# Kernel tuning notes

Hardware: AMD Instinct MI355X
Metric: run time of the kernel (lower is better)

## Reference

```python
import jax, jax.numpy as jnp
import numpy as np

EPS = 1e-8  # torch F.cosine_similarity eps


def _cos_attn_masked(x, roi, h):
    """Replicates MultiHeadedAttention_2: per-head cosine similarity, relu,
    global top-k(4) column mask (torch advanced-indexing semantics), roi mask.
    x: (B,num,C), roi: (B,num,num). Returns (B,num,num,h)."""
    B, num, C = x.shape
    dk = C // h
    xh = x.reshape(B, num, h, dk)
    n = jnp.linalg.norm(xh, axis=-1)                       # (B,num,h)
    dots = jnp.einsum('bihd,bjhd->bijh', xh, xh)           # (B,i,j,h)
    denom = jnp.maximum(n[:, :, None, :] * n[:, None, :, :], EPS)
    a = jax.nn.relu(dots / denom)                          # (B,i,j,h)
    # torch: values, idces = topk(attn, 4, dim=2); atten_mask[:, :, idces, :] = 1
    # -> column j is unmasked iff j appears ANYWHERE in idces (global union).
    _, idx = jax.lax.top_k(jnp.moveaxis(a, 2, -1), 4)      # (B,i,h,4) over j
    vec = jnp.zeros((num,), a.dtype).at[idx.reshape(-1)].set(1.0)
    return a * roi[:, :, :, None] * vec[None, None, :, None]


def _gconv_relu(x, w, b):
    """Grouped 1x1 Conv1d + ReLU. x: (B,C,num), w: (g, co_g, ci_g), b: (co,)."""
    B, C, num = x.shape
    g, co_g, ci_g = w.shape
    xg = x.reshape(B, g, ci_g, num)
    y = jnp.einsum('goc,bgcn->bgon', w, xg).reshape(B, g * co_g, num)
    return jax.nn.relu(y + b[None, :, None])


def setup_inputs() -> dict:
    key = jax.random.key(0)
    ks = jax.random.split(key, 10)
    B, num = 4, 1024
    c_in, c_mid, c_out, group = 256, 256, 256, 4
    inp = {
        'input': jax.random.normal(ks[0], (B, num, c_in), jnp.float32),
        'masks_roi': jax.random.randint(ks[1], (B, num, num), 0, 2, jnp.int32),
        'score_mask': jax.random.randint(ks[2], (B, num), 0, 2, jnp.int32),
        'gt_feat': jax.random.normal(ks[3], (B, num, c_in), jnp.float32),
        'w1': jax.random.normal(ks[4], (group, c_mid // group, c_in // group), jnp.float32) * 0.05,
        'b1': jax.random.normal(ks[5], (c_mid,), jnp.float32) * 0.05,
        'w2': jax.random.normal(ks[6], (group, c_out // group, c_mid // group), jnp.float32) * 0.05,
        'b2': jax.random.normal(ks[7], (c_out,), jnp.float32) * 0.05,
        'gt_w': jax.random.normal(ks[8], (c_out, c_in), jnp.float32) * 0.05,
        'gt_b': jax.random.normal(ks[9], (c_out,), jnp.float32) * 0.05,
        # module init explicitly zeroes LayerNorm weight AND bias
        'ln_w': jnp.zeros((c_out,), jnp.float32),
        'ln_b': jnp.zeros((c_out,), jnp.float32),
        'multi_head': 4,
    }
    return inp


def reference(input, masks_roi, score_mask, gt_feat, w1, b1, w2, b2, gt_w, gt_b, ln_w, ln_b, multi_head):
    h = multi_head
    B, num, C = input.shape
    dt = input.dtype
    sm = score_mask.astype(dt)
    roi = masks_roi.astype(dt) * sm[:, None, :]
    f_mask = jax.vmap(jnp.diag)((sm == 0).astype(dt))      # (B,num,num)

    gts = jax.nn.relu(gt_feat @ gt_w.T + gt_b).reshape(B, -1, gt_w.shape[0])

    # --- stage 1 ---
    a1 = (_cos_attn_masked(input, roi, h) + f_mask[:, :, :, None]) / 4.0
    p1 = a1.transpose(0, 3, 2, 1)                          # (B,h,j,i)
    out1 = _gconv_relu(input.transpose(0, 2, 1), w1, b1)   # (B,mid,num)
    mid = out1.shape[1]
    o1m = jnp.einsum('bhcj,bhji->bhci', out1.reshape(B, h, mid // h, num), p1)
    out1 = out1 + o1m.reshape(B, mid, num)

    # --- stage 2 ---
    a2 = (_cos_attn_masked(out1.transpose(0, 2, 1), roi, h) + f_mask[:, :, :, None]) / 4.0
    p2 = a2.transpose(0, 3, 2, 1)
    out2 = _gconv_relu(out1, w2, b2)                       # (B,out,num)
    co = out2.shape[1]
    o2m = jnp.einsum('bhcj,bhji->bhci', out2.reshape(B, h, co // h, num), p2)
    y = o2m.reshape(B, co, num).transpose(0, 2, 1)         # (B,num,out)

    # LayerNorm(eps=1e-6) -- weight/bias zero-initialized per the module
    mu = y.mean(-1, keepdims=True)
    var = y.var(-1, keepdims=True)
    node_feat = (y - mu) / jnp.sqrt(var + 1e-6) * ln_w + ln_b

    out2 = out2 + node_feat.transpose(0, 2, 1)
    return out2.transpose(0, 2, 1), gts, node_feat


if __name__ == '__main__':
    o = reference(**setup_inputs())
    print([x.shape for x in o])
```

## Files before the change

kernel.cpp:

```cpp
#include <hip/hip_runtime.h>
#include <hip/hip_bf16.h>

#define B_    4
#define NUM   1024
#define CH    256
#define HEADS 4
#define DK    64
#define LDK   72
#define NJC   4

typedef __hip_bfloat16 bf;
typedef __attribute__((ext_vector_type(8))) short short8;
typedef __attribute__((ext_vector_type(4))) float f32x4;
typedef unsigned long long u64;
typedef unsigned u32;

#define SEG_ ((size_t)B_ * NUM * CH)

__device__ inline bf tobf(float v) { return __float2bfloat16(v); }

__device__ inline void stage_tile(const float* __restrict__ src, size_t row0,
                                  int col0, int rowstride, bf (*dst)[LDK], int tid) {
  int r = tid >> 4, c4 = (tid & 15) * 4;
  #pragma unroll
  for (int it = 0; it < 4; ++it) {
    int row = r + it * 16;
    const float4 v = *(const float4*)&src[(row0 + row) * (size_t)rowstride + col0 + c4];
    union { bf h4[4]; short4 s4; } u;
    u.h4[0] = tobf(v.x); u.h4[1] = tobf(v.y); u.h4[2] = tobf(v.z); u.h4[3] = tobf(v.w);
    *(short4*)&dst[row][c4] = u.s4;
  }
}

__device__ inline void load_afrag_bf(const bf* __restrict__ arow, int quad, short8 af[2]) {
  af[0] = *(const short8*)&arow[quad * 8];
  af[1] = *(const short8*)&arow[32 + quad * 8];
}

__device__ inline u32 umax(u32 a, u32 b) { return a > b ? a : b; }
__device__ inline u32 umin(u32 a, u32 b) { return a < b ? a : b; }

__device__ inline void sort4(u32& k0, u32& k1, u32& k2, u32& k3) {
  u32 h;
  h = umax(k0, k1); k1 = umin(k0, k1); k0 = h;
  h = umax(k2, k3); k3 = umin(k2, k3); k2 = h;
  h = umax(k0, k2); k2 = umin(k0, k2); k0 = h;
  h = umax(k1, k3); k3 = umin(k1, k3); k1 = h;
  h = umax(k1, k2); k2 = umin(k1, k2); k1 = h;
}

__device__ inline void merge4(u32 t[4], u32 o0, u32 o1, u32 o2, u32 o3) {
  u32 m0 = umax(t[0], o3), m1 = umax(t[1], o2);
  u32 m2 = umax(t[2], o1), m3 = umax(t[3], o0);
  u32 h;
  h = umax(m0, m2); m2 = umin(m0, m2); m0 = h;
  h = umax(m1, m3); m3 = umin(m1, m3); m1 = h;
  h = umax(m0, m1); m1 = umin(m0, m1); m0 = h;
  h = umax(m2, m3); m3 = umin(m2, m3); m2 = h;
  t[0] = m0; t[1] = m1; t[2] = m2; t[3] = m3;
}

__device__ inline void conv_body(
    char* SM, int m0, int g, int tid,
    const float* __restrict__ x, const float* __restrict__ parts,
    const float* __restrict__ w,
    const float* __restrict__ bias, const int* __restrict__ smask,
    float seedbase, bool skipx, float* __restrict__ out, float* __restrict__ out2,
    float* __restrict__ rn, bf* __restrict__ xbf) {
  float (*Xs)[65] = (float(*)[65])SM;
  float (*Wsm)[65] = (float(*)[65])(SM + 16640);
  const int tx = tid & 15, ty = tid >> 4;
  #pragma unroll
  for (int l = 0; l < 16; ++l) {
    int idx = tid + l * 256; int r = idx >> 6, c = idx & 63;
    size_t gi = (size_t)(m0 + r) * CH + g * DK + c;
    float v = x[gi];
    if (parts)
      v += parts[gi] + parts[SEG_ + gi] + parts[2 * SEG_ + gi] + parts[3 * SEG_ + gi];
    Xs[r][c] = v;
    Wsm[r][c] = w[g * DK * DK + r * DK + c];
  }
  __syncthreads();
  if (!skipx) {
    int r = tid >> 4, c4 = (tid & 15) * 4;
    #pragma unroll
    for (int it = 0; it < 4; ++it) {
      int row = r + it * 16;
      union { bf h4[4]; short4 s4; } u;
      u.h4[0] = tobf(Xs[row][c4]);     u.h4[1] = tobf(Xs[row][c4 + 1]);
      u.h4[2] = tobf(Xs[row][c4 + 2]); u.h4[3] = tobf(Xs[row][c4 + 3]);
      *(short4*)&xbf[(size_t)(m0 + row) * CH + g * DK + c4] = u.s4;
    }
  }
  if (!skipx) {
    int wv = tid >> 6, lane = tid & 63;
    int row = wv * 16 + (lane >> 2), part = lane & 3;
    float s = 0.f;
    #pragma unroll
    for (int k = 0; k < 16; ++k) {
      float v = Xs[row][part * 16 + k];
      s += v * v;
    }
    s += __shfl_xor(s, 1, 64);
    s += __shfl_xor(s, 2, 64);
    if (part == 0)
      rn[(size_t)(m0 + row) * HEADS + g] = 1.0f / fmaxf(sqrtf(s), 1e-4f);
  }
  float acc[4][4] = {};
  #pragma unroll 8
  for (int k = 0; k < DK; ++k) {
    float av[4], bv[4];
    #pragma unroll
    for (int i = 0; i < 4; ++i) av[i] = Xs[ty * 4 + i][k];
    #pragma unroll
    for (int j = 0; j < 4; ++j) bv[j] = Wsm[tx * 4 + j][k];
    #pragma unroll
    for (int i = 0; i < 4; ++i)
      #pragma unroll
      for (int j = 0; j < 4; ++j) acc[i][j] += av[i] * bv[j];
  }
  #pragma unroll
  for (int i = 0; i < 4; ++i) {
    int row = m0 + ty * 4 + i;
    float seed = seedbase + ((smask[row] == 0) ? 0.25f : 0.f);
    #pragma unroll
    for (int j = 0; j < 4; ++j) {
      int o = g * DK + tx * 4 + j;
      size_t idx = (size_t)row * CH + o;
      float v = fmaxf(acc[i][j] + bias[o], 0.f);
      out[idx] = v;
      out2[idx] = v * seed;
    }
  }
}

__device__ inline void gts_body(
    char* SM, int m0, int n0, int tid,
    const float* __restrict__ gf, const float* __restrict__ gw,
    const float* __restrict__ gb, float* __restrict__ out) {
  bf (*As)[LDK] = (bf(*)[LDK])SM;
  bf (*Bs)[LDK] = (bf(*)[LDK])(SM + 9216);
  const int lane = tid & 63, w = tid >> 6;
  const int m = lane & 15, quad = lane >> 4;
  f32x4 acc[4] = {{0.f,0.f,0.f,0.f},{0.f,0.f,0.f,0.f},{0.f,0.f,0.f,0.f},{0.f,0.f,0.f,0.f}};
  for (int k0 = 0; k0 < 256; k0 += 64) {
    __syncthreads();
    stage_tile(gf, m0, k0, 256, As, tid);
    stage_tile(gw, n0, k0, 256, Bs, tid);
    __syncthreads();
    #pragma unroll
    for (int kb = 0; kb < 2; ++kb) {
      short8 a = *(const short8*)&As[w * 16 + m][kb * 32 + quad * 8];
      #pragma unroll
      for (int nt = 0; nt < 4; ++nt) {
        short8 bb = *(const short8*)&Bs[nt * 16 + m][kb * 32 + quad * 8];
        acc[nt] = __builtin_amdgcn_mfma_f32_16x16x32_bf16(a, bb, acc[nt], 0, 0, 0);
      }
    }
  }
  #pragma unroll
  for (int nt = 0; nt < 4; ++nt)
    #pragma unroll
    for (int r = 0; r < 4; ++r) {
      int row = m0 + w * 16 + quad * 4 + r, col = n0 + nt * 16 + m;
      out[(size_t)row * 256 + col] = fmaxf(acc[nt][r] + gb[col], 0.f);
    }
}

__device__ inline void pack_body(int blkrow, int tid, const int* __restrict__ mroi,
                                 const int* __restrict__ smask, u64* __restrict__ pk,
                                 float* __restrict__ v1, float* __restrict__ v2) {
  if (blkrow < 4) {
    int i = blkrow * 256 + tid;
    v1[i] = 0.f; v2[i] = 0.f;
  }
  int row = blkrow * 4 + (tid >> 6);
  int lane = tid & 63;
  int b = row >> 10;
  const int* mr = &mroi[(size_t)row * NUM];
  const int* sm = &smask[b * NUM];
  #pragma unroll
  for (int wd = 0; wd < 16; ++wd) {
    int j = wd * 64 + lane;
    u64 word = __ballot((mr[j] != 0) && (sm[j] != 0));
    if (lane == 0) pk[(size_t)row * 16 + wd] = word;
  }
}

__global__ __launch_bounds__(256) void head_kernel(
    const float* __restrict__ x, const float* __restrict__ w1,
    const float* __restrict__ b1, const int* __restrict__ smask,
    float* __restrict__ X1, float* __restrict__ F1, float* __restrict__ rn,
    bf* __restrict__ xbf,
    const float* __restrict__ gf, const float* __restrict__ gw,
    const float* __restrict__ gb, float* __restrict__ gts_out,
    const int* __restrict__ mroi, u64* __restrict__ pk,
    float* __restrict__ v1, float* __restrict__ v2,
    const float* __restrict__ lnw, const float* __restrict__ lnb,
    u32* __restrict__ lnz) {
  __shared__ __align__(16) char SM[33280];
  __shared__ u64 bz[4];
  const int tid = threadIdx.x;
  if (blockIdx.y < 4) {
    conv_body(SM, blockIdx.x * 64, blockIdx.y, tid, x, nullptr, w1, b1, smask,
              1.0f, false, X1, F1, rn, xbf);
  } else if (blockIdx.y < 8) {
    gts_body(SM, blockIdx.x * 64, (blockIdx.y - 4) * 64, tid, gf, gw, gb, gts_out);
  } else {
    int blkrow = (blockIdx.y - 8) * 64 + blockIdx.x;
    pack_body(blkrow, tid, mroi, smask, pk, v1, v2);
    if (blkrow == 4) {
      bool nz = (lnw[tid] != 0.f) || (lnb[tid] != 0.f);
      u64 wb = __ballot(nz);
      if ((tid & 63) == 0) bz[tid >> 6] = wb;
      __syncthreads();
      if (tid == 0) *lnz = ((bz[0] | bz[1] | bz[2] | bz[3]) == 0ull) ? 1u : 0u;
    }
  }
}

__global__ __launch_bounds__(256) void conv_kernel(
    const float* __restrict__ x, const float* __restrict__ parts,
    const float* __restrict__ w,
    const float* __restrict__ bias, const int* __restrict__ smask,
    float seedbase, float* __restrict__ out, float* __restrict__ out2,
    float* __restrict__ rn, bf* __restrict__ xbf, const u32* __restrict__ lnz) {
  __shared__ __align__(16) char SM[33280];
  bool skipx = (lnz != nullptr) && (*lnz != 0u);
  conv_body(SM, blockIdx.x * 64, blockIdx.y, threadIdx.x, x, parts, w, bias, smask,
            seedbase, skipx, out, out2, rn, xbf);
}

__global__ __launch_bounds__(1024, 4) void score_topk_kernel(
    const bf* __restrict__ xbf, const float* __restrict__ rn,
    const u64* __restrict__ pk, bf* __restrict__ wsout,
    float* __restrict__ vec, const u32* __restrict__ lnz) {
  if (lnz != nullptr && *lnz != 0u) return;
  __shared__ __align__(16) bf Xj[2][4][64][LDK];
  __shared__ u32 cexch[3][64][4];
  const int b = blockIdx.z, h = blockIdx.y, it = blockIdx.x;
  const int i0 = it * 64;
  const int tid = threadIdx.x, lane = tid & 63, wv = tid >> 6;
  const int m = lane & 15, quad = lane >> 4;
  const int g4 = wv >> 2, rw = wv & 3;
  const int slot = tid & 511, srow = slot >> 3, schunk = slot & 7;
  const int tpair = tid >> 9;

  auto sload = [&](int k, short8& n0, short8& n1) {
    size_t base = (size_t)b * NUM;
    int t0 = (tpair * 2 + 0) * 4 + k, t1 = (tpair * 2 + 1) * 4 + k;
    n0 = *(const short8*)&xbf[(base + t0 * 64 + srow) * CH + h * DK + schunk * 8];
    n1 = *(const short8*)&xbf[(base + t1 * 64 + srow) * CH + h * DK + schunk * 8];
  };
  auto swrite = [&](int buf, short8 n0, short8 n1) {
    *(short8*)&Xj[buf][tpair * 2 + 0][srow][schunk * 8] = n0;
    *(short8*)&Xj[buf][tpair * 2 + 1][srow][schunk * 8] = n1;
  };

  {
    short8 n0, n1;
    sload(0, n0, n1);
    swrite(0, n0, n1);
  }

  short8 afrag[2];
  load_afrag_bf(&xbf[((size_t)b * NUM + i0 + rw * 16 + m) * CH + h * DK], quad, afrag);

  u32 keys[4][4] = {};

  const int row0 = i0 + rw * 16 + quad * 4;
  bf* wpb = wsout + ((size_t)(b * HEADS + h) * NUM + row0) * NUM + m;
  const u64* pkb = pk + ((size_t)b * NUM + row0) * 16;
  const float* rnp = rn + ((size_t)b * NUM + m) * HEADS + h;

  __syncthreads();

  #pragma unroll
  for (int k = 0; k < 4; ++k) {
    const int cur = k & 1;
    const int jt = g4 * 4 + k;
    const int j0 = jt * 64;
    short8 n0, n1;
    if (k < 3) sload(k + 1, n0, n1);
    u64 wrm[4];
    float rnj4[4];
    #pragma unroll
    for (int r = 0; r < 4; ++r)
      wrm[r] = pkb[r * 16 + jt] >> m;
    #pragma unroll
    for (int nt = 0; nt < 4; ++nt)
      rnj4[nt] = rnp[(j0 + nt * 16) * HEADS];

    f32x4 acc[4];
    #pragma unroll
    for (int nt = 0; nt < 4; ++nt) {
      acc[nt] = (f32x4){0.f, 0.f, 0.f, 0.f};
      #pragma unroll
      for (int kb = 0; kb < 2; ++kb) {
        short8 bb = *(const short8*)&Xj[cur][g4][nt * 16 + m][kb * 32 + quad * 8];
        acc[nt] = __builtin_amdgcn_mfma_f32_16x16x32_bf16(afrag[kb], bb, acc[nt], 0, 0, 0);
      }
    }
    const u32 jinv0 = 1023u - (u32)(j0 + m);
    #pragma unroll
    for (int r = 0; r < 4; ++r) {
      float kv0 = fmaxf(acc[0][r] * rnj4[0], 0.f);
      float kv1 = fmaxf(acc[1][r] * rnj4[1], 0.f);
      float kv2 = fmaxf(acc[2][r] * rnj4[2], 0.f);
      float kv3 = fmaxf(acc[3][r] * rnj4[3], 0.f);
      u32 k0 = (__float_as_uint(kv0) & 0xFFFFFC00u) | jinv0;
      u32 k1 = (__float_as_uint(kv1) & 0xFFFFFC00u) | (jinv0 - 16u);
      u32 k2 = (__float_as_uint(kv2) & 0xFFFFFC00u) | (jinv0 - 32u);
      u32 k3 = (__float_as_uint(kv3) & 0xFFFFFC00u) | (jinv0 - 48u);
      sort4(k0, k1, k2, k3);
      merge4(keys[r], k0, k1, k2, k3);
      wpb[r * NUM + j0 +  0] = tobf((wrm[r] &        1ull) ? kv0 : 0.f);
      wpb[r * NUM + j0 + 16] = tobf((wrm[r] >> 16 &  1ull) ? kv1 : 0.f);
      wpb[r * NUM + j0 + 32] = tobf((wrm[r] >> 32 &  1ull) ? kv2 : 0.f);
      wpb[r * NUM + j0 + 48] = tobf((wrm[r] >> 48 &  1ull) ? kv3 : 0.f);
    }
    if (k < 3) swrite(cur ^ 1, n0, n1);
    __syncthreads();
  }

  #pragma unroll
  for (int st = 1; st < 16; st <<= 1) {
    #pragma unroll
    for (int r = 0; r < 4; ++r) {
      u32 o0 = (u32)__shfl_xor((int)keys[r][0], st, 64);
      u32 o1 = (u32)__shfl_xor((int)keys[r][1], st, 64);
      u32 o2 = (u32)__shfl_xor((int)keys[r][2], st, 64);
      u32 o3 = (u32)__shfl_xor((int)keys[r][3], st, 64);
      merge4(keys[r], o0, o1, o2, o3);
    }
  }
  if (g4 != 0 && m == 0) {
    #pragma unroll
    for (int r = 0; r < 4; ++r) {
      int rl = rw * 16 + quad * 4 + r;
      #pragma unroll
      for (int q = 0; q < 4; ++q) cexch[g4 - 1][rl][q] = keys[r][q];
    }
  }
  __syncthreads();
  if (g4 == 0 && m == 0) {
    #pragma unroll
    for (int r = 0; r < 4; ++r) {
      int rl = rw * 16 + quad * 4 + r;
      merge4(keys[r], cexch[0][rl][0], cexch[0][rl][1], cexch[0][rl][2], cexch[0][rl][3]);
      merge4(keys[r], cexch[1][rl][0], cexch[1][rl][1], cexch[1][rl][2], cexch[1][rl][3]);
      merge4(keys[r], cexch[2][rl][0], cexch[2][rl][1], cexch[2][rl][2], cexch[2][rl][3]);
      #pragma unroll
      for (int q = 0; q < 4; ++q)
        vec[1023u - (keys[r][q] & 0x3FFu)] = 1.0f;
    }
  }
}

__global__ __launch_bounds__(256) void pv_kernel(
    const bf* __restrict__ wsin, const float* __restrict__ conv,
    const float* __restrict__ rn, const float* __restrict__ vec,
    float* __restrict__ outp, const u32* __restrict__ lnz) {
  if (lnz != nullptr && *lnz != 0u) return;
  __shared__ __align__(16) bf Cv[2][64][LDK];
  const int b = blockIdx.z, h = blockIdx.y;
  const int it = blockIdx.x >> 2, jc = blockIdx.x & 3;
  const int i0 = it * 64, jbase = jc * 256;
  const int tid = threadIdx.x, lane = tid & 63, w = tid >> 6;
  const int m = lane & 15, quad = lane >> 4;
  const int jr = tid >> 4, c4 = tid & 15;

  float rni4[4];
  #pragma unroll
  for (int r = 0; r < 4; ++r)
    rni4[r] = 0.25f * rn[((size_t)b * NUM + i0 + w * 16 + quad * 4 + r) * HEADS + h];

  const size_t wsrow = ((size_t)(b * HEADS + h) * NUM + i0 + w * 16 + m) * NUM + jbase;

  f32x4 om[4] = {{0.f,0.f,0.f,0.f},{0.f,0.f,0.f,0.f},{0.f,0.f,0.f,0.f},{0.f,0.f,0.f,0.f}};

  float4 pre[4]; float psc[4];
  auto issue = [&](int jt) {
    #pragma unroll
    for (int itt = 0; itt < 4; ++itt) {
      int j = jbase + jt * 64 + jr + itt * 16;
      psc[itt] = vec[j];
      pre[itt] = *(const float4*)&conv[((size_t)b * NUM + j) * CH + h * DK + c4 * 4];
    }
  };
  auto lwrite = [&](int buf) {
    #pragma unroll
    for (int itt = 0; itt < 4; ++itt) {
      int j = jr + itt * 16;
      Cv[buf][c4 * 4 + 0][j] = tobf(pre[itt].x * psc[itt]);
      Cv[buf][c4 * 4 + 1][j] = tobf(pre[itt].y * psc[itt]);
      Cv[buf][c4 * 4 + 2][j] = tobf(pre[itt].z * psc[itt]);
      Cv[buf][c4 * 4 + 3][j] = tobf(pre[itt].w * psc[itt]);
    }
  };

  issue(0); lwrite(0);
  short8 a0 = *(const short8*)&wsin[wsrow + quad * 8];
  short8 a1 = *(const short8*)&wsin[wsrow + 32 + quad * 8];

  for (int jt = 0; jt < 4; ++jt) {
    const int cur = jt & 1;
    short8 na0, na1;
    if (jt < 3) {
      issue(jt + 1);
      na0 = *(const short8*)&wsin[wsrow + (jt + 1) * 64 + quad * 8];
      na1 = *(const short8*)&wsin[wsrow + (jt + 1) * 64 + 32 + quad * 8];
    }
    __syncthreads();
    #pragma unroll
    for (int ct = 0; ct < 4; ++ct)
      om[ct] = __builtin_amdgcn_mfma_f32_16x16x32_bf16(
          a0, *(const short8*)&Cv[cur][ct * 16 + m][quad * 8], om[ct], 0, 0, 0);
    #pragma unroll
    for (int ct = 0; ct < 4; ++ct)
      om[ct] = __builtin_amdgcn_mfma_f32_16x16x32_bf16(
          a1, *(const short8*)&Cv[cur][ct * 16 + m][32 + quad * 8], om[ct], 0, 0, 0);
    if (jt < 3) { lwrite(cur ^ 1); a0 = na0; a1 = na1; }
  }

  const size_t ob = (size_t)(jc * B_ + b) * NUM;
  #pragma unroll
  for (int ct = 0; ct < 4; ++ct)
    #pragma unroll
    for (int r = 0; r < 4; ++r) {
      size_t idx = (ob + i0 + w * 16 + quad * 4 + r) * CH + h * DK + ct * 16 + m;
      outp[idx] = om[ct][r] * rni4[r];
    }
}

__global__ __launch_bounds__(256) void final_kernel(
    float* __restrict__ ybnf, float* __restrict__ out0,
    const float* __restrict__ lnw, const float* __restrict__ lnb,
    const float* __restrict__ parts, const u32* __restrict__ lnz) {
  int bn = blockIdx.x;
  int c = threadIdx.x;
  size_t idx = (size_t)bn * CH + c;
  if (lnz != nullptr && *lnz != 0u) {
    ybnf[idx] = 0.f;
    return;
  }
  __shared__ float r1[4];
  __shared__ float r2[4];
  float y = ybnf[idx] + parts[idx] + parts[SEG_ + idx]
          + parts[2 * SEG_ + idx] + parts[3 * SEG_ + idx];
  float x2v = out0[idx];
  float s = y;
  #pragma unroll
  for (int off = 32; off; off >>= 1) s += __shfl_down(s, off, 64);
  int wave = c >> 6, lane = c & 63;
  if (lane == 0) r1[wave] = s;
  __syncthreads();
  float mu = (r1[0] + r1[1] + r1[2] + r1[3]) * (1.f / 256.f);
  float d = y - mu;
  float s2 = d * d;
  #pragma unroll
  for (int off = 32; off; off >>= 1) s2 += __shfl_down(s2, off, 64);
  if (lane == 0) r2[wave] = s2;
  __syncthreads();
  float var = (r2[0] + r2[1] + r2[2] + r2[3]) * (1.f / 256.f);
  float nf = d * rsqrtf(var + 1e-6f) * lnw[c] + lnb[c];
  ybnf[idx] = nf;
  out0[idx] = x2v + nf;
}

extern "C" void kernel_launch(void* const* d_in, const int* in_sizes, int n_in,
                              void* d_out, int out_size, void* d_ws, size_t ws_size,
                              hipStream_t stream) {
  const float* input = (const float*)d_in[0];
  const int* mroi = (const int*)d_in[1];
  const int* smask = (const int*)d_in[2];
  const float* gt_feat = (const float*)d_in[3];
  const float* w1 = (const float*)d_in[4];
  const float* b1 = (const float*)d_in[5];
  const float* w2 = (const float*)d_in[6];
  const float* b2 = (const float*)d_in[7];
  const float* gt_w = (const float*)d_in[8];
  const float* gt_b = (const float*)d_in[9];
  const float* lnw = (const float*)d_in[10];
  const float* lnb = (const float*)d_in[11];

  const size_t SEG = SEG_;
  float* out0 = (float*)d_out;
  float* gts = out0 + SEG;
  float* nfreg = out0 + 2 * SEG;

  float* F1 = (float*)d_ws;
  float* RN = F1 + SEG;
  float* VEC1 = RN + (size_t)B_ * NUM * HEADS;
  float* VEC2 = VEC1 + NUM;
  u64* PK = (u64*)(VEC2 + NUM);
  bf* XBF = (bf*)(PK + (size_t)B_ * NUM * 16);
  bf* WSC = XBF + SEG;
  float* P = (float*)(WSC + (size_t)B_ * HEADS * NUM * NUM);
  u32* LNZ = (u32*)(P + 4 * SEG);

  float* X1 = nfreg;
  float* X2 = out0;
  float* Yb = nfreg;

  head_kernel<<<dim3(64, 24), 256, 0, stream>>>(
      input, w1, b1, smask, X1, F1, RN, XBF,
      gt_feat, gt_w, gt_b, gts, mroi, PK, VEC1, VEC2, lnw, lnb, LNZ);

  score_topk_kernel<<<dim3(16, HEADS, B_), 1024, 0, stream>>>(
      XBF, RN, PK, WSC, VEC1, nullptr);
  pv_kernel<<<dim3(16 * NJC, HEADS, B_), 256, 0, stream>>>(WSC, X1, RN, VEC1, P, nullptr);

  conv_kernel<<<dim3(64, 4), 256, 0, stream>>>(F1, P, w2, b2, smask, 0.0f, X2, Yb, RN, XBF, LNZ);
  score_topk_kernel<<<dim3(16, HEADS, B_), 1024, 0, stream>>>(
      XBF, RN, PK, WSC, VEC2, LNZ);
  pv_kernel<<<dim3(16 * NJC, HEADS, B_), 256, 0, stream>>>(WSC, X2, RN, VEC2, P, LNZ);

  final_kernel<<<4096, 256, 0, stream>>>(Yb, X2, lnw, lnb, P, LNZ);
}
```

Before: 162.6 us.

## Stage all j-tiles in LDS upfront and drop per-iteration barriers in score_topk

The score/top-k kernel now loads all 16 j-tiles of the head slice into shared memory at once, replacing the double-buffered per-iteration loads. This removes the four per-iteration __syncthreads and the load/compute interleave, in exchange for much larger LDS use (about 147KB for Xj) and so lower occupancy, plus more live registers during the upfront load. Separately, the conv kernel skips writing out2 when the skip flag is set.

Result: slower. 166.9 us (+2.6%).

```diff
diff --git a/kernel.cpp b/kernel.cpp
--- a/kernel.cpp
+++ b/kernel.cpp
@@ -129,7 +129,7 @@
       size_t idx = (size_t)row * CH + o;
       float v = fmaxf(acc[i][j] + bias[o], 0.f);
       out[idx] = v;
-      out2[idx] = v * seed;
+      if (!skipx) out2[idx] = v * seed;
     }
   }
 }
@@ -236,7 +236,7 @@
     const u64* __restrict__ pk, bf* __restrict__ wsout,
     float* __restrict__ vec, const u32* __restrict__ lnz) {
   if (lnz != nullptr && *lnz != 0u) return;
-  __shared__ __align__(16) bf Xj[2][4][64][LDK];
+  __shared__ __align__(16) bf Xj[16][64][LDK];
   __shared__ u32 cexch[3][64][4];
   const int b = blockIdx.z, h = blockIdx.y, it = blockIdx.x;
   const int i0 = it * 64;
@@ -246,21 +246,15 @@
   const int slot = tid & 511, srow = slot >> 3, schunk = slot & 7;
   const int tpair = tid >> 9;
 
-  auto sload = [&](int k, short8& n0, short8& n1) {
-    size_t base = (size_t)b * NUM;
-    int t0 = (tpair * 2 + 0) * 4 + k, t1 = (tpair * 2 + 1) * 4 + k;
-    n0 = *(const short8*)&xbf[(base + t0 * 64 + srow) * CH + h * DK + schunk * 8];
-    n1 = *(const short8*)&xbf[(base + t1 * 64 + srow) * CH + h * DK + schunk * 8];
-  };
-  auto swrite = [&](int buf, short8 n0, short8 n1) {
-    *(short8*)&Xj[buf][tpair * 2 + 0][srow][schunk * 8] = n0;
-    *(short8*)&Xj[buf][tpair * 2 + 1][srow][schunk * 8] = n1;
-  };
-
   {
-    short8 n0, n1;
-    sload(0, n0, n1);
-    swrite(0, n0, n1);
+    short8 v[8];
+    const bf* sb = &xbf[((size_t)b * NUM + srow) * CH + h * DK + schunk * 8];
+    #pragma unroll
+    for (int q = 0; q < 8; ++q)
+      v[q] = *(const short8*)&sb[(size_t)(tpair + 2 * q) * 64 * CH];
+    #pragma unroll
+    for (int q = 0; q < 8; ++q)
+      *(short8*)&Xj[tpair + 2 * q][srow][schunk * 8] = v[q];
   }
 
   short8 afrag[2];
@@ -277,11 +271,8 @@
 
   #pragma unroll
   for (int k = 0; k < 4; ++k) {
-    const int cur = k & 1;
     const int jt = g4 * 4 + k;
     const int j0 = jt * 64;
-    short8 n0, n1;
-    if (k < 3) sload(k + 1, n0, n1);
     u64 wrm[4];
     float rnj4[4];
     #pragma unroll
@@ -297,7 +288,7 @@
       acc[nt] = (f32x4){0.f, 0.f, 0.f, 0.f};
       #pragma unroll
       for (int kb = 0; kb < 2; ++kb) {
-        short8 bb = *(const short8*)&Xj[cur][g4][nt * 16 + m][kb * 32 + quad * 8];
+        short8 bb = *(const short8*)&Xj[jt][nt * 16 + m][kb * 32 + quad * 8];
         acc[nt] = __builtin_amdgcn_mfma_f32_16x16x32_bf16(afrag[kb], bb, acc[nt], 0, 0, 0);
       }
     }
@@ -319,8 +310,6 @@
       wpb[r * NUM + j0 + 32] = tobf((wrm[r] >> 32 &  1ull) ? kv2 : 0.f);
       wpb[r * NUM + j0 + 48] = tobf((wrm[r] >> 48 &  1ull) ? kv3 : 0.f);
     }
-    if (k < 3) swrite(cur ^ 1, n0, n1);
-    __syncthreads();
   }
 
   #pragma unroll
```
